# Kernel optimization log

Hardware: AMD Instinct MI355X
Metric: run time of the kernel (lower is better)

## Reference

```python
import jax, jax.numpy as jnp
import numpy as np

N_HEAD = 16
N_KV_HEAD = 4
HEAD_DIM = 64
VE_CH = 12  # min(12, n_embd)


def apply_rotary_emb(x, cos, sin):
    d = x.shape[3] // 2
    x1, x2 = x[..., :d], x[..., d:]
    return jnp.concatenate([x1 * cos + x2 * sin, x1 * -sin + x2 * cos], axis=3)


def rms_norm(x):
    return x * jax.lax.rsqrt(jnp.mean(jnp.square(x), axis=-1, keepdims=True) + 1e-6)


def setup_inputs() -> dict:
    key = jax.random.key(0)
    ks = jax.random.split(key, 9)
    B, T, C = 2, 2048, 1024
    s = 0.02
    return {
        "x": jax.random.normal(ks[0], (B, T, C), jnp.float32),
        "ve": jax.random.normal(ks[1], (B, T, N_KV_HEAD * HEAD_DIM), jnp.float32),
        "cos": jax.random.normal(ks[2], (1, T, 1, HEAD_DIM // 2), jnp.float32),
        "sin": jax.random.normal(ks[3], (1, T, 1, HEAD_DIM // 2), jnp.float32),
        "Wq": jax.random.normal(ks[4], (C, C), jnp.float32) * s,
        "Wk": jax.random.normal(ks[5], (N_KV_HEAD * HEAD_DIM, C), jnp.float32) * s,
        "Wv": jax.random.normal(ks[6], (N_KV_HEAD * HEAD_DIM, C), jnp.float32) * s,
        "Wo": jax.random.normal(ks[7], (C, C), jnp.float32) * s,
        "Wg": jax.random.normal(ks[8], (N_KV_HEAD, VE_CH), jnp.float32) * s,
    }


def reference(x, ve, cos, sin, Wq, Wk, Wv, Wo, Wg):
    B, T, C = x.shape
    q = (x @ Wq.T).reshape(B, T, N_HEAD, HEAD_DIM)
    k = (x @ Wk.T).reshape(B, T, N_KV_HEAD, HEAD_DIM)
    v = (x @ Wv.T).reshape(B, T, N_KV_HEAD, HEAD_DIM)

    # value-embedding gate
    ve_r = ve.reshape(B, T, N_KV_HEAD, HEAD_DIM)
    gate = 3.0 * jax.nn.sigmoid(x[..., :VE_CH] @ Wg.T)  # [B,T,n_kv_head]
    v = v + gate[..., None] * ve_r

    q = apply_rotary_emb(q, cos, sin)
    k = apply_rotary_emb(k, cos, sin)
    q = rms_norm(q) * 1.2
    k = rms_norm(k) * 1.2

    # GQA: expand kv heads
    r = N_HEAD // N_KV_HEAD
    k = jnp.repeat(k, r, axis=2)
    v = jnp.repeat(v, r, axis=2)

    # [B,H,T,D]
    q = q.transpose(0, 2, 1, 3)
    k = k.transpose(0, 2, 1, 3)
    v = v.transpose(0, 2, 1, 3)

    scale = 1.0 / np.sqrt(HEAD_DIM).astype(np.float32)
    scores = jnp.einsum("bhqd,bhkd->bhqk", q, k) * scale
    causal = jnp.tril(jnp.ones((T, T), dtype=bool))
    scores = jnp.where(causal, scores, jnp.float32(-jnp.inf))
    att = jax.nn.softmax(scores, axis=-1)
    y = jnp.einsum("bhqk,bhkd->bhqd", att, v)
    y = y.transpose(0, 2, 1, 3).reshape(B, T, C)
    return y @ Wo.T
```

## Files before the change

### kernel.cpp

```cpp
#include <hip/hip_runtime.h>
#include <stdint.h>

#define B_SZ 2
#define T_SZ 2048
#define C_SZ 1024
#define NH   16
#define NKV  4
#define HD   64
#define KVD  256
#define QKV_N 1536

typedef __attribute__((ext_vector_type(8))) short bf16x8;
typedef __attribute__((ext_vector_type(4))) float f32x4;

#define GL(p) ((const __attribute__((address_space(1))) void*)(p))
#define LD(p) ((__attribute__((address_space(3))) void*)(p))

__device__ inline unsigned short f2bf(float f) {
  union { float f; unsigned u; } v; v.f = f;
  unsigned u = v.u;
  unsigned r = (u + 0x7fffu + ((u >> 16) & 1u)) >> 16;
  return (unsigned short)r;
}
__device__ inline unsigned short bftrunc(float f) {
  union { float f; unsigned u; } v; v.f = f;
  return (unsigned short)(v.u >> 16);
}

struct CvtArgs {
  const float *s0, *s1, *s2, *s3, *s4;
  unsigned short *d0, *d1, *d2, *d3, *d4;
  const float *x, *Wg;
  float *gate;
};
__global__ __launch_bounds__(256) void cvt_all(CvtArgs a) {
  int blk = blockIdx.x, tid = threadIdx.x;
  if (blk >= 6656) {
    int idx = (blk - 6656) * 256 + tid;
    int bt = idx >> 2, kh = idx & 3;
    float s = 0.f;
#pragma unroll
    for (int j = 0; j < 12; j++) s += a.x[(size_t)bt * C_SZ + j] * a.Wg[kh * 12 + j];
    a.gate[idx] = 3.f / (1.f + __expf(-s));
    return;
  }
  const float* s; unsigned short* d; int i;
  if      (blk < 4096) { s = a.s0; d = a.d0; i = blk * 256 + tid; }
  else if (blk < 5120) { s = a.s1; d = a.d1; i = (blk - 4096) * 256 + tid; }
  else if (blk < 5376) { s = a.s2; d = a.d2; i = (blk - 5120) * 256 + tid; }
  else if (blk < 5632) { s = a.s3; d = a.d3; i = (blk - 5376) * 256 + tid; }
  else                 { s = a.s4; d = a.d4; i = (blk - 5632) * 256 + tid; }
  float4 f = ((const float4*)s)[i];
  ushort4 o;
  o.x = f2bf(f.x); o.y = f2bf(f.y); o.z = f2bf(f.z); o.w = f2bf(f.w);
  ((ushort4*)d)[i] = o;
}

#define GEMM_PROLOG(A, Bm, K)                                                        \
  __shared__ unsigned short As[4][64 * 32];                                          \
  __shared__ unsigned short Bs[4][128 * 32];                                         \
  int tid  = threadIdx.x;                                                            \
  int lane = tid & 63;                                                               \
  int wave = tid >> 6;                                                               \
  int quad = lane >> 4;                                                              \
  int l16  = lane & 15;                                                              \
  int m0 = blockIdx.y * 64;                                                          \
  int n0 = blockIdx.x * 128;                                                         \
  int wm = (wave & 1) * 32;                                                          \
  int wn = (wave >> 1) * 64;                                                         \
  f32x4 acc[2][4];                                                                   \
  _Pragma("unroll") for (int i = 0; i < 2; i++)                                      \
    _Pragma("unroll") for (int j = 0; j < 4; j++)                                    \
      acc[i][j] = (f32x4){0.f, 0.f, 0.f, 0.f};                                       \
  int lrow = lane >> 2;                                                              \
  int lcol = (lane & 3) * 8;                                                         \
  int srowA = wave * 16;                                                             \
  int srowB = wave * 32;                                                             \
  const unsigned short* aP  = &A[(size_t)(m0 + srowA + lrow) * K + lcol];            \
  const unsigned short* b0P = &Bm[(size_t)(n0 + srowB + lrow) * K + lcol];           \
  const unsigned short* b1P = b0P + 16 * (size_t)K;                                  \
  for (int k0 = 0; k0 < K; k0 += 128) {                                              \
    __syncthreads();                                                                 \
    _Pragma("unroll") for (int p = 0; p < 4; p++) {                                  \
      __builtin_amdgcn_global_load_lds(GL(aP  + k0 + p * 32), LD(&As[p][srowA * 32]),        16, 0, 0); \
      __builtin_amdgcn_global_load_lds(GL(b0P + k0 + p * 32), LD(&Bs[p][srowB * 32]),        16, 0, 0); \
      __builtin_amdgcn_global_load_lds(GL(b1P + k0 + p * 32), LD(&Bs[p][(srowB + 16) * 32]), 16, 0, 0); \
    }                                                                                \
    __syncthreads();                                                                 \
    _Pragma("unroll") for (int p = 0; p < 4; p++) {                                  \
      bf16x8 af[2], bfr[4];                                                          \
      _Pragma("unroll") for (int i = 0; i < 2; i++)                                  \
        af[i] = *(const bf16x8*)&As[p][(wm + i * 16 + l16) * 32 + quad * 8];         \
      _Pragma("unroll") for (int j = 0; j < 4; j++)                                  \
        bfr[j] = *(const bf16x8*)&Bs[p][(wn + j * 16 + l16) * 32 + quad * 8];        \
      _Pragma("unroll") for (int i = 0; i < 2; i++)                                  \
        _Pragma("unroll") for (int j = 0; j < 4; j++)                                \
          acc[i][j] = __builtin_amdgcn_mfma_f32_16x16x32_bf16(af[i], bfr[j], acc[i][j], 0, 0, 0); \
    }                                                                                \
  }

__global__ __launch_bounds__(256) void gemm_bt(const unsigned short* __restrict__ A,
                                               const unsigned short* __restrict__ Bm,
                                               float* __restrict__ C,
                                               int N, int K) {
  GEMM_PROLOG(A, Bm, K)
#pragma unroll
  for (int i = 0; i < 2; i++) {
#pragma unroll
    for (int j = 0; j < 4; j++) {
      int col = n0 + wn + j * 16 + l16;
#pragma unroll
      for (int r = 0; r < 4; r++) {
        int row = m0 + wm + i * 16 + quad * 4 + r;
        C[(size_t)row * N + col] = acc[i][j][r];
      }
    }
  }
}

__global__ __launch_bounds__(256) void gemm_qkv(const unsigned short* __restrict__ A,
                                                const unsigned short* __restrict__ Bm,
                                                const float* __restrict__ ve,
                                                const float* __restrict__ cosb,
                                                const float* __restrict__ sinb,
                                                const float* __restrict__ gateArr,
                                                unsigned short* __restrict__ qa,
                                                unsigned short* __restrict__ ka,
                                                unsigned short* __restrict__ vt) {
  const int K = C_SZ;
  GEMM_PROLOG(A, Bm, K)

  int colbase = n0 + wn;
  if (colbase < 1280) {
    int isQ = colbase < 1024;
    int h   = isQ ? (colbase >> 6) : ((colbase - 1024) >> 6);
    float scale = isQ ? (0.15f * 1.44269504088896f) : 1.2f;
    unsigned short* dst = isQ ? qa : ka;
    int nheads = isQ ? NH : NKV;
#pragma unroll
    for (int i = 0; i < 2; i++) {
#pragma unroll
      for (int r = 0; r < 4; r++) {
        int row = m0 + wm + i * 16 + quad * 4 + r;
        int t = row & (T_SZ - 1), b = row >> 11;
        float a10 = acc[i][0][r], a11 = acc[i][1][r];
        float a20 = acc[i][2][r], a21 = acc[i][3][r];
        float cv0 = cosb[t * 32 + l16],      sv0 = sinb[t * 32 + l16];
        float cv1 = cosb[t * 32 + 16 + l16], sv1 = sinb[t * 32 + 16 + l16];
        float o10 =  a10 * cv0 + a20 * sv0;
        float o11 =  a11 * cv1 + a21 * sv1;
        float o20 = -a10 * sv0 + a20 * cv0;
        float o21 = -a11 * sv1 + a21 * cv1;
        float ssq = o10 * o10 + o11 * o11 + o20 * o20 + o21 * o21;
        ssq += __shfl_xor(ssq, 1);
        ssq += __shfl_xor(ssq, 2);
        ssq += __shfl_xor(ssq, 4);
        ssq += __shfl_xor(ssq, 8);
        float rn = rsqrtf(ssq * (1.f / 64.f) + 1e-6f) * scale;
        size_t base = ((size_t)(b * nheads + h) * T_SZ + t) * HD;
        dst[base + l16]      = f2bf(o10 * rn);
        dst[base + 16 + l16] = f2bf(o11 * rn);
        dst[base + 32 + l16] = f2bf(o20 * rn);
        dst[base + 48 + l16] = f2bf(o21 * rn);
      }
    }
  } else {
    int kh = (colbase - 1280) >> 6;
#pragma unroll
    for (int i = 0; i < 2; i++) {
#pragma unroll
      for (int r = 0; r < 4; r++) {
        int row = m0 + wm + i * 16 + quad * 4 + r;
        int t = row & (T_SZ - 1), b = row >> 11;
        float g = gateArr[row * 4 + kh];
        size_t vbase = ((size_t)(b * NKV + kh) * HD) * T_SZ;
#pragma unroll
        for (int j = 0; j < 4; j++) {
          int d = j * 16 + l16;
          float val = acc[i][j][r] + g * ve[(size_t)row * KVD + kh * HD + d];
          vt[vbase + (size_t)d * T_SZ + t] = f2bf(val);
        }
      }
    }
  }
}

#define KST 72
#define PST 72
__global__ __launch_bounds__(256) void attn(const unsigned short* __restrict__ qa,
                                            const unsigned short* __restrict__ ka,
                                            const unsigned short* __restrict__ vt,
                                            unsigned short* __restrict__ y) {
  int bid = blockIdx.x;
  int half = bid >> 8, r = bid & 255;
  int qt = half ? (r & 15) : 15 - (r & 15);
  int bh = (half << 4) | (r >> 4);
  int b = bh >> 4, h = bh & 15;
  int kh = h >> 2;
  int tid = threadIdx.x;
  int wave = tid >> 6, lane = tid & 63;
  int quad = lane >> 4, l16 = lane & 15;

  __shared__ unsigned short Ks[64 * KST];
  __shared__ unsigned short Vs[64 * KST];
  __shared__ unsigned short Ps[128 * PST];
  unsigned short* Pw = &Ps[(wave * 32) * PST];

  bf16x8 bq[2][2];
#pragma unroll
  for (int qi = 0; qi < 2; qi++) {
    int tq = qt * 128 + wave * 32 + qi * 16 + l16;
    const unsigned short* qp = &qa[((size_t)(b * NH + h) * T_SZ + tq) * HD];
    bq[qi][0] = *(const bf16x8*)&qp[quad * 8];
    bq[qi][1] = *(const bf16x8*)&qp[32 + quad * 8];
  }

  const unsigned short one_bf = 0x3F80;
  bf16x8 vones = {(short)one_bf, (short)one_bf, (short)one_bf, (short)one_bf,
                  (short)one_bf, (short)one_bf, (short)one_bf, (short)one_bf};

  f32x4 oacc[2][4];
  f32x4 lacc[2];
#pragma unroll
  for (int qi = 0; qi < 2; qi++) {
    lacc[qi] = (f32x4){0.f, 0.f, 0.f, 0.f};
#pragma unroll
    for (int d = 0; d < 4; d++) oacc[qi][d] = (f32x4){0.f, 0.f, 0.f, 0.f};
  }

  int lr = tid >> 2;
  int lc = (tid & 3) * 16;

  const unsigned short* kbase = &ka[(size_t)(b * NKV + kh) * T_SZ * HD];
  const unsigned short* vbase = &vt[(size_t)(b * NKV + kh) * HD * T_SZ];

  int nj = 2 * qt + 2;

  uint4 k0, k1, v0, v1;
  {
    const unsigned short* kp = &kbase[(size_t)lr * HD + lc];
    const unsigned short* vp = &vbase[(size_t)lr * T_SZ + lc];
    k0 = *(const uint4*)(kp);
    k1 = *(const uint4*)(kp + 8);
    v0 = *(const uint4*)(vp);
    v1 = *(const uint4*)(vp + 8);
  }

  int qrow0 = qt * 128 + wave * 32;

  for (int j = 0; j < nj; j++) {
    __syncthreads();
    *(uint4*)&Ks[lr * KST + lc]     = k0;
    *(uint4*)&Ks[lr * KST + lc + 8] = k1;
    *(uint4*)&Vs[lr * KST + lc]     = v0;
    *(uint4*)&Vs[lr * KST + lc + 8] = v1;
    __syncthreads();

    if (j + 1 < nj) {
      const unsigned short* kp = &kbase[(size_t)((j + 1) * 64 + lr) * HD + lc];
      const unsigned short* vp = &vbase[(size_t)lr * T_SZ + (j + 1) * 64 + lc];
      k0 = *(const uint4*)(kp);
      k1 = *(const uint4*)(kp + 8);
      v0 = *(const uint4*)(vp);
      v1 = *(const uint4*)(vp + 8);
    }

    f32x4 st[4][2];
#pragma unroll
    for (int tb = 0; tb < 4; tb++) {
      bf16x8 ak0 = *(const bf16x8*)&Ks[(tb * 16 + l16) * KST + quad * 8];
      bf16x8 ak1 = *(const bf16x8*)&Ks[(tb * 16 + l16) * KST + 32 + quad * 8];
#pragma unroll
      for (int qi = 0; qi < 2; qi++) {
        f32x4 s = (f32x4){0.f, 0.f, 0.f, 0.f};
        s = __builtin_amdgcn_mfma_f32_16x16x32_bf16(ak0, bq[qi][0], s, 0, 0, 0);
        s = __builtin_amdgcn_mfma_f32_16x16x32_bf16(ak1, bq[qi][1], s, 0, 0, 0);
        st[tb][qi] = s;
      }
    }

#pragma unroll
    for (int qi = 0; qi < 2; qi++) {
      int qlow = qrow0 + qi * 16;
      if (j * 64 + 63 > qlow) {
        int qg = qlow + l16;
#pragma unroll
        for (int tb = 0; tb < 4; tb++) {
          int tg = j * 64 + tb * 16 + quad * 4;
#pragma unroll
          for (int i = 0; i < 4; i++) {
            if (tg + i > qg) st[tb][qi][i] = -__builtin_inff();
          }
        }
      }
#pragma unroll
      for (int tb = 0; tb < 4; tb++) {
        ushort4 w;
        w.x = bftrunc(__builtin_amdgcn_exp2f(st[tb][qi][0]));
        w.y = bftrunc(__builtin_amdgcn_exp2f(st[tb][qi][1]));
        w.z = bftrunc(__builtin_amdgcn_exp2f(st[tb][qi][2]));
        w.w = bftrunc(__builtin_amdgcn_exp2f(st[tb][qi][3]));
        *(ushort4*)&Pw[(qi * 16 + l16) * PST + tb * 16 + quad * 4] = w;
      }
    }

    bf16x8 ap[2][2];
#pragma unroll
    for (int qi = 0; qi < 2; qi++) {
      ap[qi][0] = *(const bf16x8*)&Pw[(qi * 16 + l16) * PST + quad * 8];
      ap[qi][1] = *(const bf16x8*)&Pw[(qi * 16 + l16) * PST + 32 + quad * 8];
      lacc[qi] = __builtin_amdgcn_mfma_f32_16x16x32_bf16(ap[qi][0], vones, lacc[qi], 0, 0, 0);
      lacc[qi] = __builtin_amdgcn_mfma_f32_16x16x32_bf16(ap[qi][1], vones, lacc[qi], 0, 0, 0);
    }
#pragma unroll
    for (int d = 0; d < 4; d++) {
      bf16x8 bv0 = *(const bf16x8*)&Vs[(d * 16 + l16) * KST + quad * 8];
      bf16x8 bv1 = *(const bf16x8*)&Vs[(d * 16 + l16) * KST + 32 + quad * 8];
#pragma unroll
      for (int qi = 0; qi < 2; qi++) {
        oacc[qi][d] = __builtin_amdgcn_mfma_f32_16x16x32_bf16(ap[qi][0], bv0, oacc[qi][d], 0, 0, 0);
        oacc[qi][d] = __builtin_amdgcn_mfma_f32_16x16x32_bf16(ap[qi][1], bv1, oacc[qi][d], 0, 0, 0);
      }
    }
  }

#pragma unroll
  for (int qi = 0; qi < 2; qi++) {
#pragma unroll
    for (int i = 0; i < 4; i++) {
      int tq = qrow0 + qi * 16 + quad * 4 + i;
      float inv = 1.f / lacc[qi][i];
#pragma unroll
      for (int d = 0; d < 4; d++) {
        y[((size_t)(b * T_SZ) + tq) * C_SZ + h * HD + d * 16 + l16] = f2bf(oacc[qi][d][i] * inv);
      }
    }
  }
}

extern "C" void kernel_launch(void* const* d_in, const int* in_sizes, int n_in,
                              void* d_out, int out_size, void* d_ws, size_t ws_size,
                              hipStream_t stream) {
  const float* x    = (const float*)d_in[0];
  const float* ve   = (const float*)d_in[1];
  const float* cosb = (const float*)d_in[2];
  const float* sinb = (const float*)d_in[3];
  const float* Wq   = (const float*)d_in[4];
  const float* Wk   = (const float*)d_in[5];
  const float* Wv   = (const float*)d_in[6];
  const float* Wo   = (const float*)d_in[7];
  const float* Wg   = (const float*)d_in[8];
  float* out = (float*)d_out;

  const size_t MB = 1024 * 1024;
  char* ws = (char*)d_ws;
  unsigned short* xb    = (unsigned short*)(ws);
  unsigned short* wqkvb = (unsigned short*)(ws + 8 * MB);
  unsigned short* wob   = (unsigned short*)(ws + 11 * MB);
  unsigned short* qab   = (unsigned short*)(ws + 13 * MB);
  unsigned short* kab   = (unsigned short*)(ws + 21 * MB);
  unsigned short* vtb   = (unsigned short*)(ws + 23 * MB);
  float*          gateA = (float*)(ws + 25 * MB);
  unsigned short* yb    = xb;

  CvtArgs ca;
  ca.s0 = x;  ca.d0 = xb;
  ca.s1 = Wq; ca.d1 = wqkvb;
  ca.s2 = Wk; ca.d2 = wqkvb + 1024 * 1024;
  ca.s3 = Wv; ca.d3 = wqkvb + 1280 * 1024;
  ca.s4 = Wo; ca.d4 = wob;
  ca.x = x; ca.Wg = Wg; ca.gate = gateA;
  cvt_all<<<6720, 256, 0, stream>>>(ca);

  gemm_qkv<<<dim3(QKV_N / 128, (B_SZ * T_SZ) / 64), 256, 0, stream>>>(
      xb, wqkvb, ve, cosb, sinb, gateA, qab, kab, vtb);

  attn<<<512, 256, 0, stream>>>(qab, kab, vtb, yb);

  gemm_bt<<<dim3(C_SZ / 128, (B_SZ * T_SZ) / 64), 256, 0, stream>>>(
      yb, wob, out, C_SZ, C_SZ);
}
```

Measured before the change: 172.0 us.

## Split long causal attention tiles across KV halves and merge partials

```diff
diff --git a/kernel.cpp b/kernel.cpp
--- a/kernel.cpp
+++ b/kernel.cpp
@@ -187,14 +187,21 @@
 
 #define KST 72
 #define PST 72
+#define PUNIT 8320
 __global__ __launch_bounds__(256) void attn(const unsigned short* __restrict__ qa,
                                             const unsigned short* __restrict__ ka,
                                             const unsigned short* __restrict__ vt,
-                                            unsigned short* __restrict__ y) {
+                                            unsigned short* __restrict__ y,
+                                            float* __restrict__ pbuf) {
+  const int U_QT[24] = {15,15,7,14,14,6,13,13,12,12,5,11,11,10,10,4,9,9,8,8,3,2,1,0};
+  const int U_J0[24] = {0,16,0,0,15,0,0,14,0,13,0,0,12,0,11,0,0,10,0,9,0,0,0,0};
+  const int U_J1[24] = {16,32,16,15,30,14,14,28,13,26,12,12,24,11,22,10,10,20,9,18,8,6,4,2};
+
   int bid = blockIdx.x;
-  int half = bid >> 8, r = bid & 255;
-  int qt = half ? (r & 15) : 15 - (r & 15);
-  int bh = (half << 4) | (r >> 4);
+  int u = bid >> 5, bh = bid & 31;
+  int qt = U_QT[u], j0 = U_J0[u], j1 = U_J1[u];
+  int split = (qt >= 8);
+  int part = (j0 != 0) ? 1 : 0;
   int b = bh >> 4, h = bh & 15;
   int kh = h >> 2;
   int tid = threadIdx.x;
@@ -234,12 +241,10 @@
   const unsigned short* kbase = &ka[(size_t)(b * NKV + kh) * T_SZ * HD];
   const unsigned short* vbase = &vt[(size_t)(b * NKV + kh) * HD * T_SZ];
 
-  int nj = 2 * qt + 2;
-
   uint4 k0, k1, v0, v1;
   {
-    const unsigned short* kp = &kbase[(size_t)lr * HD + lc];
-    const unsigned short* vp = &vbase[(size_t)lr * T_SZ + lc];
+    const unsigned short* kp = &kbase[(size_t)(j0 * 64 + lr) * HD + lc];
+    const unsigned short* vp = &vbase[(size_t)lr * T_SZ + j0 * 64 + lc];
     k0 = *(const uint4*)(kp);
     k1 = *(const uint4*)(kp + 8);
     v0 = *(const uint4*)(vp);
@@ -248,7 +253,7 @@
 
   int qrow0 = qt * 128 + wave * 32;
 
-  for (int j = 0; j < nj; j++) {
+  for (int j = j0; j < j1; j++) {
     __syncthreads();
     *(uint4*)&Ks[lr * KST + lc]     = k0;
     *(uint4*)&Ks[lr * KST + lc + 8] = k1;
@@ -256,7 +261,7 @@
     *(uint4*)&Vs[lr * KST + lc + 8] = v1;
     __syncthreads();
 
-    if (j + 1 < nj) {
+    if (j + 1 < j1) {
       const unsigned short* kp = &kbase[(size_t)((j + 1) * 64 + lr) * HD + lc];
       const unsigned short* vp = &vbase[(size_t)lr * T_SZ + (j + 1) * 64 + lc];
       k0 = *(const uint4*)(kp);
@@ -324,17 +329,50 @@
     }
   }
 
-#pragma unroll
-  for (int qi = 0; qi < 2; qi++) {
-#pragma unroll
-    for (int i = 0; i < 4; i++) {
-      int tq = qrow0 + qi * 16 + quad * 4 + i;
-      float inv = 1.f / lacc[qi][i];
-#pragma unroll
-      for (int d = 0; d < 4; d++) {
-        y[((size_t)(b * T_SZ) + tq) * C_SZ + h * HD + d * 16 + l16] = f2bf(oacc[qi][d][i] * inv);
-      }
-    }
+  if (split) {
+    float* pb = &pbuf[(size_t)(((bh * 8 + (qt - 8)) * 2 + part)) * PUNIT];
+#pragma unroll
+    for (int qi = 0; qi < 2; qi++) {
+#pragma unroll
+      for (int i = 0; i < 4; i++) {
+        int row = wave * 32 + qi * 16 + quad * 4 + i;
+#pragma unroll
+        for (int d = 0; d < 4; d++)
+          pb[row * 64 + d * 16 + l16] = oacc[qi][d][i];
+        if (l16 == 0) pb[8192 + row] = lacc[qi][i];
+      }
+    }
+  } else {
+#pragma unroll
+    for (int qi = 0; qi < 2; qi++) {
+#pragma unroll
+      for (int i = 0; i < 4; i++) {
+        int tq = qrow0 + qi * 16 + quad * 4 + i;
+        float inv = 1.f / lacc[qi][i];
+#pragma unroll
+        for (int d = 0; d < 4; d++) {
+          y[((size_t)(b * T_SZ) + tq) * C_SZ + h * HD + d * 16 + l16] = f2bf(oacc[qi][d][i] * inv);
+        }
+      }
+    }
+  }
+}
+
+__global__ __launch_bounds__(256) void attn_merge(const float* __restrict__ pbuf,
+                                                  unsigned short* __restrict__ y) {
+  int unit = blockIdx.x;
+  int bh = unit >> 3, qt = (unit & 7) + 8;
+  int b = bh >> 4, h = bh & 15;
+  const float* p0 = &pbuf[(size_t)(unit * 2) * PUNIT];
+  const float* p1 = p0 + PUNIT;
+  int d = threadIdx.x & 63;
+  int r0 = (threadIdx.x >> 6) * 32;
+#pragma unroll 4
+  for (int r = r0; r < r0 + 32; r++) {
+    float l = p0[8192 + r] + p1[8192 + r];
+    float o = p0[r * 64 + d] + p1[r * 64 + d];
+    int t = qt * 128 + r;
+    y[((size_t)(b * T_SZ) + t) * C_SZ + h * HD + d] = f2bf(o * (1.f / l));
   }
 }
 
@@ -361,6 +399,7 @@
   unsigned short* kab   = (unsigned short*)(ws + 21 * MB);
   unsigned short* vtb   = (unsigned short*)(ws + 23 * MB);
   float*          gateA = (float*)(ws + 25 * MB);
+  float*          pbuf  = (float*)(ws + 26 * MB);
   unsigned short* yb    = xb;
 
   CvtArgs ca;
@@ -375,7 +414,9 @@
   gemm_qkv<<<dim3(QKV_N / 128, (B_SZ * T_SZ) / 64), 256, 0, stream>>>(
       xb, wqkvb, ve, cosb, sinb, gateA, qab, kab, vtb);
 
-  attn<<<512, 256, 0, stream>>>(qab, kab, vtb, yb);
+  attn<<<768, 256, 0, stream>>>(qab, kab, vtb, yb, pbuf);
+
+  attn_merge<<<256, 256, 0, stream>>>(pbuf, yb);
 
   gemm_bt<<<dim3(C_SZ / 128, (B_SZ * T_SZ) / 64), 256, 0, stream>>>(
       yb, wob, out, C_SZ, C_SZ);
```

New measurement: 177.9 us. 3.4% more time.

## Double-buffer K/V tiles in attention and transpose V in separate kernel

Applied to the files above, without the earlier changes.

```diff
diff --git a/kernel.cpp b/kernel.cpp
--- a/kernel.cpp
+++ b/kernel.cpp
@@ -126,7 +126,7 @@
                                                 const float* __restrict__ gateArr,
                                                 unsigned short* __restrict__ qa,
                                                 unsigned short* __restrict__ ka,
-                                                unsigned short* __restrict__ vt) {
+                                                unsigned short* __restrict__ vtmp) {
   const int K = C_SZ;
   GEMM_PROLOG(A, Bm, K)
 
@@ -171,18 +171,48 @@
 #pragma unroll
       for (int r = 0; r < 4; r++) {
         int row = m0 + wm + i * 16 + quad * 4 + r;
-        int t = row & (T_SZ - 1), b = row >> 11;
         float g = gateArr[row * 4 + kh];
-        size_t vbase = ((size_t)(b * NKV + kh) * HD) * T_SZ;
 #pragma unroll
         for (int j = 0; j < 4; j++) {
           int d = j * 16 + l16;
           float val = acc[i][j][r] + g * ve[(size_t)row * KVD + kh * HD + d];
-          vt[vbase + (size_t)d * T_SZ + t] = f2bf(val);
+          vtmp[(size_t)row * KVD + kh * HD + d] = f2bf(val);
         }
       }
     }
   }
+}
+
+__global__ __launch_bounds__(256) void v_transpose(const unsigned short* __restrict__ vtmp,
+                                                   unsigned short* __restrict__ vt) {
+  __shared__ unsigned short tile[64 * 68];
+  int blk = blockIdx.x;
+  int tb = blk & 31, kh = (blk >> 5) & 3, b = blk >> 7;
+  int tid = threadIdx.x;
+  int r = tid >> 2, c = (tid & 3) * 16;
+  const unsigned short* src = &vtmp[((size_t)(b * T_SZ + tb * 64 + r)) * KVD + kh * HD + c];
+  uint4 x0 = *(const uint4*)(src);
+  uint4 x1 = *(const uint4*)(src + 8);
+  *(uint2*)&tile[r * 68 + c]      = *(uint2*)&x0;
+  *(uint2*)&tile[r * 68 + c + 4]  = *((uint2*)&x0 + 1);
+  *(uint2*)&tile[r * 68 + c + 8]  = *(uint2*)&x1;
+  *(uint2*)&tile[r * 68 + c + 12] = *((uint2*)&x1 + 1);
+  __syncthreads();
+  int d = tid >> 2, tc = (tid & 3) * 16;
+  ushort4 o0, o1, o2, o3;
+  o0.x = tile[(tc + 0) * 68 + d];  o0.y = tile[(tc + 1) * 68 + d];
+  o0.z = tile[(tc + 2) * 68 + d];  o0.w = tile[(tc + 3) * 68 + d];
+  o1.x = tile[(tc + 4) * 68 + d];  o1.y = tile[(tc + 5) * 68 + d];
+  o1.z = tile[(tc + 6) * 68 + d];  o1.w = tile[(tc + 7) * 68 + d];
+  o2.x = tile[(tc + 8) * 68 + d];  o2.y = tile[(tc + 9) * 68 + d];
+  o2.z = tile[(tc + 10) * 68 + d]; o2.w = tile[(tc + 11) * 68 + d];
+  o3.x = tile[(tc + 12) * 68 + d]; o3.y = tile[(tc + 13) * 68 + d];
+  o3.z = tile[(tc + 14) * 68 + d]; o3.w = tile[(tc + 15) * 68 + d];
+  unsigned short* dst = &vt[((size_t)(b * NKV + kh) * HD + d) * T_SZ + tb * 64 + tc];
+  *(ushort4*)(dst)      = o0;
+  *(ushort4*)(dst + 4)  = o1;
+  *(ushort4*)(dst + 8)  = o2;
+  *(ushort4*)(dst + 12) = o3;
 }
 
 #define KST 72
@@ -201,8 +231,8 @@
   int wave = tid >> 6, lane = tid & 63;
   int quad = lane >> 4, l16 = lane & 15;
 
-  __shared__ unsigned short Ks[64 * KST];
-  __shared__ unsigned short Vs[64 * KST];
+  __shared__ unsigned short Ks[2][64 * KST];
+  __shared__ unsigned short Vs[2][64 * KST];
   __shared__ unsigned short Ps[128 * PST];
   unsigned short* Pw = &Ps[(wave * 32) * PST];
 
@@ -236,27 +266,28 @@
 
   int nj = 2 * qt + 2;
 
-  uint4 k0, k1, v0, v1;
   {
     const unsigned short* kp = &kbase[(size_t)lr * HD + lc];
     const unsigned short* vp = &vbase[(size_t)lr * T_SZ + lc];
-    k0 = *(const uint4*)(kp);
-    k1 = *(const uint4*)(kp + 8);
-    v0 = *(const uint4*)(vp);
-    v1 = *(const uint4*)(vp + 8);
+    uint4 k0 = *(const uint4*)(kp);
+    uint4 k1 = *(const uint4*)(kp + 8);
+    uint4 v0 = *(const uint4*)(vp);
+    uint4 v1 = *(const uint4*)(vp + 8);
+    *(uint4*)&Ks[0][lr * KST + lc]     = k0;
+    *(uint4*)&Ks[0][lr * KST + lc + 8] = k1;
+    *(uint4*)&Vs[0][lr * KST + lc]     = v0;
+    *(uint4*)&Vs[0][lr * KST + lc + 8] = v1;
   }
 
   int qrow0 = qt * 128 + wave * 32;
 
   for (int j = 0; j < nj; j++) {
+    int cur = j & 1, nxt = cur ^ 1;
     __syncthreads();
-    *(uint4*)&Ks[lr * KST + lc]     = k0;
-    *(uint4*)&Ks[lr * KST + lc + 8] = k1;
-    *(uint4*)&Vs[lr * KST + lc]     = v0;
-    *(uint4*)&Vs[lr * KST + lc + 8] = v1;
-    __syncthreads();
-
-    if (j + 1 < nj) {
+
+    uint4 k0, k1, v0, v1;
+    bool pf = (j + 1 < nj);
+    if (pf) {
       const unsigned short* kp = &kbase[(size_t)((j + 1) * 64 + lr) * HD + lc];
       const unsigned short* vp = &vbase[(size_t)lr * T_SZ + (j + 1) * 64 + lc];
       k0 = *(const uint4*)(kp);
@@ -268,8 +299,8 @@
     f32x4 st[4][2];
 #pragma unroll
     for (int tb = 0; tb < 4; tb++) {
-      bf16x8 ak0 = *(const bf16x8*)&Ks[(tb * 16 + l16) * KST + quad * 8];
-      bf16x8 ak1 = *(const bf16x8*)&Ks[(tb * 16 + l16) * KST + 32 + quad * 8];
+      bf16x8 ak0 = *(const bf16x8*)&Ks[cur][(tb * 16 + l16) * KST + quad * 8];
+      bf16x8 ak1 = *(const bf16x8*)&Ks[cur][(tb * 16 + l16) * KST + 32 + quad * 8];
 #pragma unroll
       for (int qi = 0; qi < 2; qi++) {
         f32x4 s = (f32x4){0.f, 0.f, 0.f, 0.f};
@@ -314,13 +345,20 @@
     }
 #pragma unroll
     for (int d = 0; d < 4; d++) {
-      bf16x8 bv0 = *(const bf16x8*)&Vs[(d * 16 + l16) * KST + quad * 8];
-      bf16x8 bv1 = *(const bf16x8*)&Vs[(d * 16 + l16) * KST + 32 + quad * 8];
+      bf16x8 bv0 = *(const bf16x8*)&Vs[cur][(d * 16 + l16) * KST + quad * 8];
+      bf16x8 bv1 = *(const bf16x8*)&Vs[cur][(d * 16 + l16) * KST + 32 + quad * 8];
 #pragma unroll
       for (int qi = 0; qi < 2; qi++) {
         oacc[qi][d] = __builtin_amdgcn_mfma_f32_16x16x32_bf16(ap[qi][0], bv0, oacc[qi][d], 0, 0, 0);
         oacc[qi][d] = __builtin_amdgcn_mfma_f32_16x16x32_bf16(ap[qi][1], bv1, oacc[qi][d], 0, 0, 0);
       }
+    }
+
+    if (pf) {
+      *(uint4*)&Ks[nxt][lr * KST + lc]     = k0;
+      *(uint4*)&Ks[nxt][lr * KST + lc + 8] = k1;
+      *(uint4*)&Vs[nxt][lr * KST + lc]     = v0;
+      *(uint4*)&Vs[nxt][lr * KST + lc + 8] = v1;
     }
   }
 
@@ -361,6 +399,7 @@
   unsigned short* kab   = (unsigned short*)(ws + 21 * MB);
   unsigned short* vtb   = (unsigned short*)(ws + 23 * MB);
   float*          gateA = (float*)(ws + 25 * MB);
+  unsigned short* vtmp  = (unsigned short*)(ws + 26 * MB);
   unsigned short* yb    = xb;
 
   CvtArgs ca;
@@ -373,7 +412,9 @@
   cvt_all<<<6720, 256, 0, stream>>>(ca);
 
   gemm_qkv<<<dim3(QKV_N / 128, (B_SZ * T_SZ) / 64), 256, 0, stream>>>(
-      xb, wqkvb, ve, cosb, sinb, gateA, qab, kab, vtb);
+      xb, wqkvb, ve, cosb, sinb, gateA, qab, kab, vtmp);
+
+  v_transpose<<<256, 256, 0, stream>>>(vtmp, vtb);
 
   attn<<<512, 256, 0, stream>>>(qab, kab, vtb, yb);
 
```

After: 172.7 us. About the same (+0.4%).
